# Kernel tuning notes

Hardware: AMD Instinct MI355X
Metric: run time of the kernel (lower is better)

The kernel has to match this reference:

```python
import jax, jax.numpy as jnp
import numpy as np

B, N, FEAT, HID, HEADS = 16, 1024, 512, 1024, 2

def setup_inputs() -> dict:
    key = jax.random.key(0)
    ks = jax.random.split(key, 20)
    s = 0.03
    d = {
        'Fs':  jax.random.normal(ks[0], (B, N, FEAT), jnp.float32),
        'Fq':  jax.random.normal(ks[1], (B, N, FEAT), jnp.float32),
        'Fms': jax.random.normal(ks[2], (B, N, FEAT), jnp.float32),
        'out_dim': N,
        'W1': jax.random.normal(ks[3], (FEAT, FEAT), jnp.float32) * s,
        'W2': jax.random.normal(ks[4], (FEAT, FEAT), jnp.float32) * s,
        'W3': jax.random.normal(ks[5], (FEAT, FEAT), jnp.float32) * s,
        'W4': jax.random.normal(ks[6], (FEAT, FEAT), jnp.float32) * s,
        'W5': jax.random.normal(ks[7], (FEAT, FEAT), jnp.float32) * s,
        'W6': jax.random.normal(ks[8], (FEAT, FEAT), jnp.float32) * s,
        'Wq': jax.random.normal(ks[9], (N, N), jnp.float32) * s,
        'Wk': jax.random.normal(ks[10], (N, N), jnp.float32) * s,
        'Wv': jax.random.normal(ks[11], (N, N), jnp.float32) * s,
        'ln_g': jnp.ones((N,), jnp.float32),
        'ln_b': jnp.zeros((N,), jnp.float32),
        'ffn_w1': jax.random.normal(ks[12], (N, HID), jnp.float32) * s,
        'ffn_w2': jax.random.normal(ks[13], (HID, N), jnp.float32) * s,
        'ffn_ln_g': jnp.ones((N,), jnp.float32),
        'ffn_ln_b': jnp.zeros((N,), jnp.float32),
    }
    return d

def _layernorm(x, g, b, eps):
    mu = x.mean(-1, keepdims=True)
    var = x.var(-1, keepdims=True)
    return (x - mu) * jax.lax.rsqrt(var + eps) * g + b

def _affinity(a, b, Wa, Wb, cl):
    # softmax((a Wa)(b Wb)^T / sqrt(cl)) over last axis
    s = jnp.einsum('bnc,bmc->bnm', a @ Wa, b @ Wb) / jnp.sqrt(jnp.float32(cl))
    return jax.nn.softmax(s, axis=-1)

def reference(Fs, Fq, Fms, out_dim, W1, W2, W3, W4, W5, W6, Wq, Wk, Wv,
              ln_g, ln_b, ffn_w1, ffn_w2, ffn_ln_g, ffn_ln_b):
    ass = _affinity(Fms, Fms, W1, W2, Fms.shape[2])   # [B,N,N]
    asq = _affinity(Fs, Fq, W3, W4, Fs.shape[2])      # [B,N,N]
    aqq = _affinity(Fq, Fq, W5, W6, Fq.shape[2])      # [B,N,N]

    Q, K, V = asq @ Wq, ass @ Wk, asq @ Wv            # [B,N,C], C=N
    Bb, Nn, C = Q.shape
    g = C // HEADS
    def heads(x):
        return x.reshape(Bb, Nn, HEADS, g).transpose(0, 2, 1, 3)  # [B,h,N,g]
    Qs, Ks, Vs = heads(Q), heads(K), heads(V)
    attn = jax.nn.softmax(jnp.einsum('bhqg,bhkg->bhqk', Qs, Ks) / jnp.sqrt(jnp.float32(g)), axis=-1)
    o = jnp.einsum('bhqk,bhkg->bhqg', attn, Vs)
    o = o.transpose(0, 2, 1, 3).reshape(Bb, Nn, C)

    x = _layernorm(o + aqq, ln_g, ln_b, 1e-5)
    y = jnp.maximum(x @ ffn_w1, 0.0) @ ffn_w2 + x     # dropout = identity (eval)
    y = _layernorm(y, ffn_ln_g, ffn_ln_b, 1e-6)
    return y
```

## Files before the change

### kernel.cpp

```cpp
#include <hip/hip_runtime.h>
#include <cstdint>

static constexpr long long Bb = 16, Nn = 1024, FE = 512;
static constexpr long long BN = Bb * Nn;
static constexpr long long E1e = BN * FE;
static constexpr long long E2n = BN * Nn;

static constexpr long long O_WT  = 0;
static constexpr long long SZ_W512 = FE * FE * 2;
static constexpr long long O_WQT = O_WT + 6 * SZ_W512;
static constexpr long long SZ_W1K = Nn * Nn * 2;
static constexpr long long O_WKT = O_WQT + SZ_W1K;
static constexpr long long O_WVT = O_WKT + SZ_W1K;
static constexpr long long O_F1T = O_WVT + SZ_W1K;
static constexpr long long O_F2T = O_F1T + SZ_W1K;
static constexpr long long O_SLOTS = O_F2T + SZ_W1K;
static constexpr long long SLOT = E2n * 2;
static constexpr long long O_S0 = O_SLOTS;
static constexpr long long O_S1 = O_S0 + SLOT;
static constexpr long long O_S2 = O_S1 + SLOT;
static constexpr long long O_E0 = O_S2 + SLOT;
static constexpr long long O_E1 = O_E0 + SLOT;
static constexpr long long O_E2 = O_E1 + SLOT;
static constexpr long long WS_NEED = O_E2 + SLOT;
static constexpr long long O_FB = O_E0;
static constexpr long long O_GT = O_S2;

typedef __attribute__((ext_vector_type(8))) short short8;
typedef __attribute__((ext_vector_type(4))) float f32x4;

static __device__ __forceinline__ unsigned short f2bf(float f) {
  union { float f; unsigned u; } x; x.f = f;
  unsigned r = x.u + 0x7FFFu + ((x.u >> 16) & 1u);
  return (unsigned short)(r >> 16);
}
static __device__ __forceinline__ float bf2f(unsigned short h) {
  union { unsigned u; float f; } x; x.u = ((unsigned)h) << 16; return x.f;
}
static __device__ __forceinline__ void gload16(const void* g, void* l) {
  __builtin_amdgcn_global_load_lds(
      (const __attribute__((address_space(1))) unsigned int*)g,
      (__attribute__((address_space(3))) unsigned int*)l, 16, 0, 0);
}

template <int EP>
__global__ __launch_bounds__(512, 2) void gemm256(
    const unsigned short* __restrict__ A, long long sA, long long hA, int lda,
    const unsigned short* __restrict__ B, long long sB, long long hB, int ldb,
    void* __restrict__ Cv, long long sC, long long hC, int ldc,
    const void* __restrict__ Rv, long long sR, int K) {
  extern __shared__ unsigned short lds[];
  const int tid = threadIdx.x;
  const int lane = tid & 63;
  const int wave = tid >> 6;
  const int wm = wave >> 2, wn = wave & 3;
  const int lrow = lane & 15, quad = lane >> 4;

  const int gx = gridDim.x;
  const int nxy = gx * gridDim.y;
  const int nwg = nxy * gridDim.z;
  int wg = blockIdx.x + gx * blockIdx.y + nxy * blockIdx.z;
  {
    const int q = nwg >> 3, r = nwg & 7;
    const int xcd = wg & 7, blk = wg >> 3;
    wg = (xcd < r ? xcd * (q + 1) : r * (q + 1) + (xcd - r) * q) + blk;
  }
  const int bz = wg / nxy;
  const int rem = wg - bz * nxy;
  const int by = rem / gx;
  const int bx = rem - by * gx;
  const int z1 = bz & 15, z2 = bz >> 4;

  const long long bm = (long long)bx * 256;
  const long long bn = (long long)by * 256;
  const unsigned short* Ab = A + z1 * sA + z2 * hA + bm * lda;
  const unsigned short* Bp = B + z1 * sB + z2 * hB + bn * ldb;

  const int srow = tid >> 2;
  const int scol = ((tid & 3) ^ ((tid >> 3) & 3)) * 8;
  unsigned short* ldst = lds + tid * 8;

  const int swq = (quad ^ ((lrow >> 1) & 3)) * 8;
  const int a_off = (wm * 128 + lrow) * 32 + swq;
  const int b_off = 8192 + (wn * 64 + lrow) * 32 + swq;

  f32x4 acc[8][4];
#pragma unroll
  for (int m = 0; m < 8; ++m)
#pragma unroll
    for (int n = 0; n < 4; ++n) acc[m][n] = (f32x4){0.f, 0.f, 0.f, 0.f};

  short8 af[8], bfr[4];
  auto READ_A0 = [&](int tt) {
    const unsigned short* lb = lds + (tt & 3) * 16384;
    bfr[0] = *(const short8*)&lb[b_off + 0 * 512];
    bfr[1] = *(const short8*)&lb[b_off + 1 * 512];
    bfr[2] = *(const short8*)&lb[b_off + 2 * 512];
    bfr[3] = *(const short8*)&lb[b_off + 3 * 512];
#pragma unroll
    for (int m = 0; m < 4; ++m) af[m] = *(const short8*)&lb[a_off + m * 512];
  };
  auto READ_A1 = [&](int tt) {
    const unsigned short* lb = lds + (tt & 3) * 16384;
#pragma unroll
    for (int m = 4; m < 8; ++m) af[m] = *(const short8*)&lb[a_off + m * 512];
  };
  auto MFMA_H = [&](int m0) {
    __builtin_amdgcn_s_setprio(1);
#pragma unroll
    for (int m = m0; m < m0 + 4; ++m)
#pragma unroll
      for (int n = 0; n < 4; ++n)
        acc[m][n] = __builtin_amdgcn_mfma_f32_16x16x32_bf16(af[m], bfr[n], acc[m][n], 0, 0, 0);
    __builtin_amdgcn_s_setprio(0);
  };
  auto STAGE = [&](int tt) {
    unsigned short* d = ldst + (tt & 3) * 16384;
    const long long ko = (long long)tt * 32 + scol;
    gload16(Ab + (long long)srow * lda + ko, d);
    gload16(Ab + (long long)(srow + 128) * lda + ko, d + 4096);
    gload16(Bp + (long long)srow * ldb + ko, d + 8192);
    gload16(Bp + (long long)(srow + 128) * ldb + ko, d + 12288);
  };

  const int nt = K >> 5;
  STAGE(0); STAGE(1); STAGE(2);
  asm volatile("s_waitcnt vmcnt(8)" ::: "memory");
  __builtin_amdgcn_s_barrier();
  int t = 0;
  for (; t < nt - 3; ++t) {
    unsigned short* d = ldst + ((t + 3) & 3) * 16384;
    const long long ko = (long long)(t + 3) * 32 + scol;
    READ_A0(t);
    gload16(Ab + (long long)srow * lda + ko, d);
    gload16(Ab + (long long)(srow + 128) * lda + ko, d + 4096);
    __builtin_amdgcn_s_barrier();
    MFMA_H(0);
    __builtin_amdgcn_s_barrier();
    READ_A1(t);
    gload16(Bp + (long long)srow * ldb + ko, d + 8192);
    gload16(Bp + (long long)(srow + 128) * ldb + ko, d + 12288);
    asm volatile("s_waitcnt vmcnt(8)" ::: "memory");
    __builtin_amdgcn_s_barrier();
    MFMA_H(4);
    __builtin_amdgcn_s_barrier();
  }
  READ_A0(t);
  __builtin_amdgcn_s_barrier();
  MFMA_H(0);
  __builtin_amdgcn_s_barrier();
  READ_A1(t);
  asm volatile("s_waitcnt vmcnt(4)" ::: "memory");
  __builtin_amdgcn_s_barrier();
  MFMA_H(4);
  __builtin_amdgcn_s_barrier();
  ++t;
  READ_A0(t);
  __builtin_amdgcn_s_barrier();
  MFMA_H(0);
  __builtin_amdgcn_s_barrier();
  READ_A1(t);
  asm volatile("s_waitcnt vmcnt(0)" ::: "memory");
  __builtin_amdgcn_s_barrier();
  MFMA_H(4);
  __builtin_amdgcn_s_barrier();
  ++t;
  READ_A0(t);
  MFMA_H(0);
  READ_A1(t);
  MFMA_H(4);

  const long long cm = bm + wm * 128, cn = bn + wn * 64;
  const long long cz = z1 * sC + z2 * hC;
#pragma unroll
  for (int mt = 0; mt < 8; ++mt) {
#pragma unroll
    for (int ntl = 0; ntl < 4; ++ntl) {
      long long col = cn + ntl * 16 + lrow;
      long long row0 = cm + mt * 16 + quad * 4;
#pragma unroll
      for (int r = 0; r < 4; ++r) {
        long long row = row0 + r;
        float v = acc[mt][ntl][r];
        long long idx = cz + row * ldc + col;
        if (EP == 1) ((unsigned short*)Cv)[idx] = f2bf(v);
        else if (EP == 2) ((unsigned short*)Cv)[idx] = f2bf(v > 0.f ? v : 0.f);
        else {
          float rr = bf2f(((const unsigned short*)Rv)[z1 * sR + row * ldc + col]);
          ((float*)Cv)[idx] = v + rr;
        }
      }
    }
  }
}

__global__ __launch_bounds__(256) void cast3_k(const float* __restrict__ i0,
                                               const float* __restrict__ i1,
                                               const float* __restrict__ i2,
                                               unsigned short* o0, unsigned short* o1,
                                               unsigned short* o2) {
  const float* in = (blockIdx.y == 0) ? i0 : (blockIdx.y == 1) ? i1 : i2;
  unsigned short* out = (blockIdx.y == 0) ? o0 : (blockIdx.y == 1) ? o1 : o2;
  long long i = (long long)blockIdx.x * 256 + threadIdx.x;
  float4 v = ((const float4*)in)[i];
  ushort4 o; o.x = f2bf(v.x); o.y = f2bf(v.y); o.z = f2bf(v.z); o.w = f2bf(v.w);
  ((ushort4*)out)[i] = o;
}

__global__ __launch_bounds__(256) void tcast6_k(const float* p0, const float* p1,
                                                const float* p2, const float* p3,
                                                const float* p4, const float* p5,
                                                unsigned short* outb, int rows, int cols) {
  const float* src[6] = {p0, p1, p2, p3, p4, p5};
  const float* in = src[blockIdx.z];
  unsigned short* out = outb + (long long)blockIdx.z * rows * cols;
  __shared__ float t[32][33];
  const int c0 = blockIdx.x * 32, r0 = blockIdx.y * 32;
  const int tx = threadIdx.x, ty = threadIdx.y;
#pragma unroll
  for (int i = 0; i < 4; ++i) {
    int r = r0 + ty + i * 8;
    t[ty + i * 8][tx] = in[(long long)r * cols + c0 + tx];
  }
  __syncthreads();
#pragma unroll
  for (int i = 0; i < 4; ++i) {
    int c = c0 + ty + i * 8;
    out[(long long)c * rows + r0 + tx] = f2bf(t[tx][ty + i * 8]);
  }
}

__global__ __launch_bounds__(256) void softmax_bf(unsigned short* __restrict__ S, float scale) {
  __shared__ float redA[4], redB[4];
  const long long row = blockIdx.x;
  const int t = threadIdx.x, wave = t >> 6, lane = t & 63;
  ushort4 u = ((ushort4*)(S + row * 1024))[t];
  float v0 = bf2f(u.x) * scale, v1 = bf2f(u.y) * scale, v2 = bf2f(u.z) * scale, v3 = bf2f(u.w) * scale;
  float m = fmaxf(fmaxf(v0, v1), fmaxf(v2, v3));
#pragma unroll
  for (int o = 32; o; o >>= 1) m = fmaxf(m, __shfl_down(m, o));
  if (lane == 0) redA[wave] = m;
  __syncthreads();
  m = fmaxf(fmaxf(redA[0], redA[1]), fmaxf(redA[2], redA[3]));
  float e0 = __expf(v0 - m), e1 = __expf(v1 - m), e2 = __expf(v2 - m), e3 = __expf(v3 - m);
  float s = e0 + e1 + e2 + e3;
#pragma unroll
  for (int o = 32; o; o >>= 1) s += __shfl_down(s, o);
  if (lane == 0) redB[wave] = s;
  __syncthreads();
  s = redB[0] + redB[1] + redB[2] + redB[3];
  float inv = 1.f / s;
  ushort4 ob; ob.x = f2bf(e0 * inv); ob.y = f2bf(e1 * inv); ob.z = f2bf(e2 * inv); ob.w = f2bf(e3 * inv);
  ((ushort4*)(S + row * 1024))[t] = ob;
}

__global__ __launch_bounds__(256) void ln1_k(const unsigned short* __restrict__ O,
                                             const unsigned short* __restrict__ Aq,
                                             const float* __restrict__ g, const float* __restrict__ b,
                                             unsigned short* __restrict__ xb) {
  __shared__ float redA[4], redB[4];
  const long long row = blockIdx.x;
  const int t = threadIdx.x, wave = t >> 6, lane = t & 63;
  ushort4 ou = ((const ushort4*)(O + row * 1024))[t];
  ushort4 au = ((const ushort4*)(Aq + row * 1024))[t];
  float v0 = bf2f(ou.x) + bf2f(au.x), v1 = bf2f(ou.y) + bf2f(au.y);
  float v2 = bf2f(ou.z) + bf2f(au.z), v3 = bf2f(ou.w) + bf2f(au.w);
  float s = v0 + v1 + v2 + v3;
  float q = v0 * v0 + v1 * v1 + v2 * v2 + v3 * v3;
#pragma unroll
  for (int o = 32; o; o >>= 1) { s += __shfl_down(s, o); q += __shfl_down(q, o); }
  if (lane == 0) { redA[wave] = s; redB[wave] = q; }
  __syncthreads();
  float S = redA[0] + redA[1] + redA[2] + redA[3];
  float Q = redB[0] + redB[1] + redB[2] + redB[3];
  float mu = S * (1.f / 1024.f);
  float var = Q * (1.f / 1024.f) - mu * mu;
  float rs = rsqrtf(var + 1e-5f);
  float4 gg = ((const float4*)g)[t], bbv = ((const float4*)b)[t];
  ushort4 ob;
  ob.x = f2bf((v0 - mu) * rs * gg.x + bbv.x);
  ob.y = f2bf((v1 - mu) * rs * gg.y + bbv.y);
  ob.z = f2bf((v2 - mu) * rs * gg.z + bbv.z);
  ob.w = f2bf((v3 - mu) * rs * gg.w + bbv.w);
  ((ushort4*)(xb + row * 1024))[t] = ob;
}

__global__ __launch_bounds__(256) void ln2_k(const float* __restrict__ Y,
                                             const float* __restrict__ g, const float* __restrict__ b,
                                             float* __restrict__ out, float eps) {
  __shared__ float redA[4], redB[4];
  const long long row = blockIdx.x;
  const int t = threadIdx.x, wave = t >> 6, lane = t & 63;
  float4 v = ((const float4*)(Y + row * 1024))[t];
  float s = v.x + v.y + v.z + v.w;
  float q = v.x * v.x + v.y * v.y + v.z * v.z + v.w * v.w;
#pragma unroll
  for (int o = 32; o; o >>= 1) { s += __shfl_down(s, o); q += __shfl_down(q, o); }
  if (lane == 0) { redA[wave] = s; redB[wave] = q; }
  __syncthreads();
  float S = redA[0] + redA[1] + redA[2] + redA[3];
  float Q = redB[0] + redB[1] + redB[2] + redB[3];
  float mu = S * (1.f / 1024.f);
  float var = Q * (1.f / 1024.f) - mu * mu;
  float rs = rsqrtf(var + eps);
  float4 gg = ((const float4*)g)[t], bbv = ((const float4*)b)[t];
  float4 o;
  o.x = (v.x - mu) * rs * gg.x + bbv.x;
  o.y = (v.y - mu) * rs * gg.y + bbv.y;
  o.z = (v.z - mu) * rs * gg.z + bbv.z;
  o.w = (v.w - mu) * rs * gg.w + bbv.w;
  ((float4*)(out + row * 1024))[t] = o;
}

extern "C" void kernel_launch(void* const* d_in, const int* in_sizes, int n_in,
                              void* d_out, int out_size, void* d_ws, size_t ws_size,
                              hipStream_t stream) {
  (void)in_sizes; (void)n_in; (void)out_size;
  if (ws_size < (size_t)WS_NEED) return;

  static int attr_once = []() {
    (void)hipFuncSetAttribute(reinterpret_cast<const void*>(&gemm256<1>),
                              hipFuncAttributeMaxDynamicSharedMemorySize, 131072);
    (void)hipFuncSetAttribute(reinterpret_cast<const void*>(&gemm256<2>),
                              hipFuncAttributeMaxDynamicSharedMemorySize, 131072);
    (void)hipFuncSetAttribute(reinterpret_cast<const void*>(&gemm256<3>),
                              hipFuncAttributeMaxDynamicSharedMemorySize, 131072);
    return 0;
  }();
  (void)attr_once;

  const float* Fs  = (const float*)d_in[0];
  const float* Fq  = (const float*)d_in[1];
  const float* Fms = (const float*)d_in[2];
  const float* Wm[6] = {(const float*)d_in[4], (const float*)d_in[5], (const float*)d_in[6],
                        (const float*)d_in[7], (const float*)d_in[8], (const float*)d_in[9]};
  const float* Wq = (const float*)d_in[10];
  const float* Wk = (const float*)d_in[11];
  const float* Wv = (const float*)d_in[12];
  const float* ln_g = (const float*)d_in[13];
  const float* ln_b = (const float*)d_in[14];
  const float* fw1 = (const float*)d_in[15];
  const float* fw2 = (const float*)d_in[16];
  const float* fg = (const float*)d_in[17];
  const float* fb = (const float*)d_in[18];
  float* out = (float*)d_out;
  uint8_t* ws = (uint8_t*)d_ws;
  auto U16 = [&](long long off) { return (unsigned short*)(ws + off); };

  const float inv_sqrt512 = 0.04419417382415922f;
  dim3 blk(256);

  auto gemm = [&](int ep, const unsigned short* A, long long sA, long long hA, int lda,
                  const unsigned short* B, long long sB, long long hB, int ldb,
                  void* C, long long sC, long long hC, int ldc, const void* R, long long sR,
                  int M, int N, int K, int batch) {
    dim3 g(M / 256, N / 256, batch);
    dim3 b(512);
    switch (ep) {
      case 1: gemm256<1><<<g, b, 131072, stream>>>(A, sA, hA, lda, B, sB, hB, ldb, C, sC, hC, ldc, R, sR, K); break;
      case 2: gemm256<2><<<g, b, 131072, stream>>>(A, sA, hA, lda, B, sB, hB, ldb, C, sC, hC, ldc, R, sR, K); break;
      default: gemm256<3><<<g, b, 131072, stream>>>(A, sA, hA, lda, B, sB, hB, ldb, C, sC, hC, ldc, R, sR, K); break;
    }
  };

  unsigned short* Wc = U16(O_WT);
  cast3_k<<<dim3(256, 3), blk, 0, stream>>>(Wm[0], Wm[1], Wm[2], Wc, Wc + 262144, Wc + 2 * 262144);
  cast3_k<<<dim3(256, 3), blk, 0, stream>>>(Wm[3], Wm[4], Wm[5], Wc + 3 * 262144, Wc + 4 * 262144, Wc + 5 * 262144);
  tcast6_k<<<dim3(32, 32, 5), dim3(32, 8), 0, stream>>>(
      Wq, Wk, Wv, fw1, fw2, fw2 , U16(O_WQT), 1024, 1024);
  unsigned short* FB = U16(O_FB);
  cast3_k<<<dim3(E1e / 4 / 256, 3), blk, 0, stream>>>(
      Fms, Fs, Fq, FB, FB + E1e, FB + 2 * E1e);

  gemm(1, Wc + 262144, 524288, 0, 512, Wc, 524288, 0, 512,
       U16(O_GT), 262144, 0, 512, nullptr, 0, 512, 512, 512, 3);
  gemm(1, FB, E1e, 0, 512, U16(O_GT), 262144, 0, 512,
       U16(O_S0), E1e, 0, 512, nullptr, 0, (int)BN, 512, 512, 3);
  gemm(1, U16(O_S0), Nn * 512, 0, 512, FB, Nn * 512, 0, 512,
       U16(O_E2), Nn * Nn, 0, 1024, nullptr, 0, 1024, 1024, 512, (int)Bb);
  gemm(1, U16(O_S0) + E1e, Nn * 512, E1e, 512, FB + 2 * E1e, Nn * 512, 0, 512,
       U16(O_E0), Nn * Nn, -(long long)E2n, 1024, nullptr, 0, 1024, 1024, 512, 32);
  softmax_bf<<<dim3(2 * BN), blk, 0, stream>>>(U16(O_S2), inv_sqrt512);
  softmax_bf<<<dim3(BN), blk, 0, stream>>>(U16(O_E2), inv_sqrt512);

  gemm(1, U16(O_E2), Nn * Nn, -(long long)(2 * E2n), 1024,
       U16(O_WKT), 0, -(long long)(SZ_W1K / 2), 1024,
       U16(O_S1), Nn * 1024, -(long long)E2n, 1024,
       nullptr, 0, 1024, 1024, 1024, 32);
  gemm(1, U16(O_WVT), 0, 0, 1024, U16(O_E0), Nn * Nn, 0, 1024, U16(O_E1), Nn * Nn, 0, 1024,
       nullptr, 0, 1024, 1024, 1024, (int)Bb);

  gemm(1, U16(O_S0), Nn * 1024, 512, 1024, U16(O_S1), Nn * 1024, 512, 1024,
       U16(O_E2), Nn * Nn, -(long long)(2 * E2n), 1024, nullptr, 0, 1024, 1024, 512, 32);
  softmax_bf<<<dim3(BN), blk, 0, stream>>>(U16(O_E2), inv_sqrt512);
  softmax_bf<<<dim3(BN), blk, 0, stream>>>(U16(O_E0), inv_sqrt512);

  gemm(1, U16(O_E2), Nn * Nn, -(long long)(2 * E2n), 1024,
       U16(O_E1), Nn * Nn, (long long)(512 * 1024), 1024,
       U16(O_S0), Nn * 1024, 512, 1024, nullptr, 0, 1024, 512, 1024, 32);

  ln1_k<<<dim3(BN), blk, 0, stream>>>(U16(O_S0), U16(O_S2), ln_g, ln_b, U16(O_S1));

  gemm(2, U16(O_S1), 0, 0, 1024, U16(O_F1T), 0, 0, 1024, U16(O_S2), 0, 0, 1024,
       nullptr, 0, (int)BN, 1024, 1024, 1);

  gemm(3, U16(O_S2), 0, 0, 1024, U16(O_F2T), 0, 0, 1024, out, 0, 0, 1024,
       U16(O_S1), 0, (int)BN, 1024, 1024, 1);

  ln2_k<<<dim3(BN), blk, 0, stream>>>(out, fg, fb, out, 1e-6f);
}
```

Before: 702.5 us.

## Switch GEMM core to 32x32x16 MFMA with split-K double-buffered register pipeline

Replaces the 16x16x32 bf16 MFMA tiling with 32x32x16 instructions, using 4x2 accumulator tiles per wave instead of 8x4. The K=32 step is split into two halves held in separate register sets, so LDS reads of one half overlap the MFMAs of the other. This cuts the number of barriers per iteration from four to one. The aim is fewer LDS reads per FLOP and less synchronization. The risks are correctness of the new swizzle and output row mapping, and register pressure from holding both register sets.

```diff
diff --git a/kernel.cpp b/kernel.cpp
--- a/kernel.cpp
+++ b/kernel.cpp
@@ -27,7 +27,7 @@
 static constexpr long long O_GT = O_S2;
 
 typedef __attribute__((ext_vector_type(8))) short short8;
-typedef __attribute__((ext_vector_type(4))) float f32x4;
+typedef __attribute__((ext_vector_type(16))) float f32x16;
 
 static __device__ __forceinline__ unsigned short f2bf(float f) {
   union { float f; unsigned u; } x; x.f = f;
@@ -54,7 +54,7 @@
   const int lane = tid & 63;
   const int wave = tid >> 6;
   const int wm = wave >> 2, wn = wave & 3;
-  const int lrow = lane & 15, quad = lane >> 4;
+  const int l31 = lane & 31, lh = lane >> 5;
 
   const int gx = gridDim.x;
   const int nxy = gx * gridDim.y;
@@ -79,41 +79,6 @@
   const int srow = tid >> 2;
   const int scol = ((tid & 3) ^ ((tid >> 3) & 3)) * 8;
   unsigned short* ldst = lds + tid * 8;
-
-  const int swq = (quad ^ ((lrow >> 1) & 3)) * 8;
-  const int a_off = (wm * 128 + lrow) * 32 + swq;
-  const int b_off = 8192 + (wn * 64 + lrow) * 32 + swq;
-
-  f32x4 acc[8][4];
-#pragma unroll
-  for (int m = 0; m < 8; ++m)
-#pragma unroll
-    for (int n = 0; n < 4; ++n) acc[m][n] = (f32x4){0.f, 0.f, 0.f, 0.f};
-
-  short8 af[8], bfr[4];
-  auto READ_A0 = [&](int tt) {
-    const unsigned short* lb = lds + (tt & 3) * 16384;
-    bfr[0] = *(const short8*)&lb[b_off + 0 * 512];
-    bfr[1] = *(const short8*)&lb[b_off + 1 * 512];
-    bfr[2] = *(const short8*)&lb[b_off + 2 * 512];
-    bfr[3] = *(const short8*)&lb[b_off + 3 * 512];
-#pragma unroll
-    for (int m = 0; m < 4; ++m) af[m] = *(const short8*)&lb[a_off + m * 512];
-  };
-  auto READ_A1 = [&](int tt) {
-    const unsigned short* lb = lds + (tt & 3) * 16384;
-#pragma unroll
-    for (int m = 4; m < 8; ++m) af[m] = *(const short8*)&lb[a_off + m * 512];
-  };
-  auto MFMA_H = [&](int m0) {
-    __builtin_amdgcn_s_setprio(1);
-#pragma unroll
-    for (int m = m0; m < m0 + 4; ++m)
-#pragma unroll
-      for (int n = 0; n < 4; ++n)
-        acc[m][n] = __builtin_amdgcn_mfma_f32_16x16x32_bf16(af[m], bfr[n], acc[m][n], 0, 0, 0);
-    __builtin_amdgcn_s_setprio(0);
-  };
   auto STAGE = [&](int tt) {
     unsigned short* d = ldst + (tt & 3) * 16384;
     const long long ko = (long long)tt * 32 + scol;
@@ -123,65 +88,94 @@
     gload16(Bp + (long long)(srow + 128) * ldb + ko, d + 12288);
   };
 
+  const int swz = (l31 >> 1) & 3;
+  const int arow = (wm * 128 + l31) * 32;
+  const int brow = 8192 + (wn * 64 + l31) * 32;
+  const int aoff0 = arow + ((0 + lh) ^ swz) * 8;
+  const int aoff1 = arow + ((2 + lh) ^ swz) * 8;
+  const int boff0 = brow + ((0 + lh) ^ swz) * 8;
+  const int boff1 = brow + ((2 + lh) ^ swz) * 8;
+
+  f32x16 acc[4][2];
+#pragma unroll
+  for (int mi = 0; mi < 4; ++mi)
+#pragma unroll
+    for (int ni = 0; ni < 2; ++ni)
+      acc[mi][ni] = (f32x16){0.f, 0.f, 0.f, 0.f, 0.f, 0.f, 0.f, 0.f,
+                             0.f, 0.f, 0.f, 0.f, 0.f, 0.f, 0.f, 0.f};
+
+  short8 a0[4], b0[2], a1[4], b1[2];
+  auto READ0 = [&](int tt) {
+    const unsigned short* lb = lds + (tt & 3) * 16384;
+#pragma unroll
+    for (int mi = 0; mi < 4; ++mi) a0[mi] = *(const short8*)&lb[aoff0 + mi * 1024];
+    b0[0] = *(const short8*)&lb[boff0];
+    b0[1] = *(const short8*)&lb[boff0 + 1024];
+  };
+  auto READ1 = [&](int tt) {
+    const unsigned short* lb = lds + (tt & 3) * 16384;
+#pragma unroll
+    for (int mi = 0; mi < 4; ++mi) a1[mi] = *(const short8*)&lb[aoff1 + mi * 1024];
+    b1[0] = *(const short8*)&lb[boff1];
+    b1[1] = *(const short8*)&lb[boff1 + 1024];
+  };
+  auto MFMA8 = [&](const short8* a, const short8* b) {
+    __builtin_amdgcn_s_setprio(1);
+#pragma unroll
+    for (int mi = 0; mi < 4; ++mi)
+#pragma unroll
+      for (int ni = 0; ni < 2; ++ni)
+        acc[mi][ni] = __builtin_amdgcn_mfma_f32_32x32x16_bf16(a[mi], b[ni], acc[mi][ni], 0, 0, 0);
+    __builtin_amdgcn_s_setprio(0);
+  };
+
   const int nt = K >> 5;
   STAGE(0); STAGE(1); STAGE(2);
   asm volatile("s_waitcnt vmcnt(8)" ::: "memory");
   __builtin_amdgcn_s_barrier();
+  READ0(0);
   int t = 0;
   for (; t < nt - 3; ++t) {
-    unsigned short* d = ldst + ((t + 3) & 3) * 16384;
-    const long long ko = (long long)(t + 3) * 32 + scol;
-    READ_A0(t);
-    gload16(Ab + (long long)srow * lda + ko, d);
-    gload16(Ab + (long long)(srow + 128) * lda + ko, d + 4096);
+    READ1(t);
+    MFMA8(a0, b0);
+    STAGE(t + 3);
+    asm volatile("s_waitcnt vmcnt(8)" ::: "memory");
+    asm volatile("s_waitcnt lgkmcnt(0)" ::: "memory");
     __builtin_amdgcn_s_barrier();
-    MFMA_H(0);
-    __builtin_amdgcn_s_barrier();
-    READ_A1(t);
-    gload16(Bp + (long long)srow * ldb + ko, d + 8192);
-    gload16(Bp + (long long)(srow + 128) * ldb + ko, d + 12288);
-    asm volatile("s_waitcnt vmcnt(8)" ::: "memory");
-    __builtin_amdgcn_s_barrier();
-    MFMA_H(4);
-    __builtin_amdgcn_s_barrier();
+    READ0(t + 1);
+    MFMA8(a1, b1);
   }
-  READ_A0(t);
+  READ1(t);
+  MFMA8(a0, b0);
+  asm volatile("s_waitcnt vmcnt(4)" ::: "memory");
+  asm volatile("s_waitcnt lgkmcnt(0)" ::: "memory");
   __builtin_amdgcn_s_barrier();
-  MFMA_H(0);
+  READ0(t + 1);
+  MFMA8(a1, b1);
+  ++t;
+  READ1(t);
+  MFMA8(a0, b0);
+  asm volatile("s_waitcnt vmcnt(0)" ::: "memory");
+  asm volatile("s_waitcnt lgkmcnt(0)" ::: "memory");
   __builtin_amdgcn_s_barrier();
-  READ_A1(t);
-  asm volatile("s_waitcnt vmcnt(4)" ::: "memory");
-  __builtin_amdgcn_s_barrier();
-  MFMA_H(4);
-  __builtin_amdgcn_s_barrier();
+  READ0(t + 1);
+  MFMA8(a1, b1);
   ++t;
-  READ_A0(t);
-  __builtin_amdgcn_s_barrier();
-  MFMA_H(0);
-  __builtin_amdgcn_s_barrier();
-  READ_A1(t);
-  asm volatile("s_waitcnt vmcnt(0)" ::: "memory");
-  __builtin_amdgcn_s_barrier();
-  MFMA_H(4);
-  __builtin_amdgcn_s_barrier();
-  ++t;
-  READ_A0(t);
-  MFMA_H(0);
-  READ_A1(t);
-  MFMA_H(4);
+  READ1(t);
+  MFMA8(a0, b0);
+  MFMA8(a1, b1);
 
   const long long cm = bm + wm * 128, cn = bn + wn * 64;
   const long long cz = z1 * sC + z2 * hC;
 #pragma unroll
-  for (int mt = 0; mt < 8; ++mt) {
-#pragma unroll
-    for (int ntl = 0; ntl < 4; ++ntl) {
-      long long col = cn + ntl * 16 + lrow;
-      long long row0 = cm + mt * 16 + quad * 4;
-#pragma unroll
-      for (int r = 0; r < 4; ++r) {
-        long long row = row0 + r;
-        float v = acc[mt][ntl][r];
+  for (int mi = 0; mi < 4; ++mi) {
+#pragma unroll
+    for (int ni = 0; ni < 2; ++ni) {
+      long long col = cn + ni * 32 + l31;
+#pragma unroll
+      for (int reg = 0; reg < 16; ++reg) {
+        long long row = cm + mi * 32 + (reg & 3) + 8 * (reg >> 2) + 4 * lh;
+        float v = acc[mi][ni][reg];
         long long idx = cz + row * ldc + col;
         if (EP == 1) ((unsigned short*)Cv)[idx] = f2bf(v);
         else if (EP == 2) ((unsigned short*)Cv)[idx] = f2bf(v > 0.f ? v : 0.f);
```

New measurement: 719.4 us. +2.4%, slower.
